# Kernel optimization log

Measured on AMD Instinct MI355X. Metric: run time of the kernel, lower is better.

The kernel has to match this reference:

```python
import jax, jax.numpy as jnp
from jax import lax
import numpy as np


def _lstm_layer(x, W_ih, W_hh, b_ih, b_hh):
    # x: (T, B, in_dim); gate order i, f, g, o (PyTorch convention)
    T, B, _ = x.shape
    H = W_hh.shape[1]
    # precompute input projections for all timesteps (one big GEMM)
    x_proj = jnp.einsum('tbi,gi->tbg', x, W_ih) + b_ih + b_hh  # (T, B, 4H)

    def step(carry, xt):
        h, c = carry
        gates = xt + h @ W_hh.T  # (B, 4H)
        i, f, g, o = jnp.split(gates, 4, axis=-1)
        c = jax.nn.sigmoid(f) * c + jax.nn.sigmoid(i) * jnp.tanh(g)
        h = jax.nn.sigmoid(o) * jnp.tanh(c)
        return (h, c), h

    h0 = jnp.zeros((B, H), dtype=x.dtype)
    c0 = jnp.zeros((B, H), dtype=x.dtype)
    (hT, cT), hs = lax.scan(step, (h0, c0), x_proj)
    return hs, hT, cT


def setup_inputs() -> dict:
    key = jax.random.key(0)
    ks = jax.random.split(key, 12)
    T, B, D_in, H, D_out = 1024, 64, 256, 512, 256
    s_in = 1.0 / np.sqrt(H)
    inp = {
        'x': jax.random.normal(ks[0], (T, B, D_in), jnp.float32),
        'W_ih0': jax.random.uniform(ks[1], (4 * H, D_in), jnp.float32, -s_in, s_in),
        'W_hh0': jax.random.uniform(ks[2], (4 * H, H), jnp.float32, -s_in, s_in),
        'b_ih0': jax.random.uniform(ks[3], (4 * H,), jnp.float32, -s_in, s_in),
        'b_hh0': jax.random.uniform(ks[4], (4 * H,), jnp.float32, -s_in, s_in),
        'W_ih1': jax.random.uniform(ks[5], (4 * H, H), jnp.float32, -s_in, s_in),
        'W_hh1': jax.random.uniform(ks[6], (4 * H, H), jnp.float32, -s_in, s_in),
        'b_ih1': jax.random.uniform(ks[7], (4 * H,), jnp.float32, -s_in, s_in),
        'b_hh1': jax.random.uniform(ks[8], (4 * H,), jnp.float32, -s_in, s_in),
        'W_out': jax.random.uniform(ks[9], (D_out, H), jnp.float32, -s_in, s_in),
        'b_out': jax.random.uniform(ks[10], (D_out,), jnp.float32, -s_in, s_in),
    }
    return inp


def reference(x, W_ih0, W_hh0, b_ih0, b_hh0, W_ih1, W_hh1, b_ih1, b_hh1, W_out, b_out):
    h1s, h1, c1 = _lstm_layer(x, W_ih0, W_hh0, b_ih0, b_hh0)
    h2s, h2, c2 = _lstm_layer(h1s, W_ih1, W_hh1, b_ih1, b_hh1)
    out = jnp.einsum('tbh,oh->tbo', h2s, W_out) + b_out  # (T, B, D_out)
    hn = jnp.stack([h1, h2], axis=0)  # (num_layers, B, H)
    cn = jnp.stack([c1, c2], axis=0)
    return (out, hn, cn)
```

## Files before the change

kernel.cpp:

```cpp
#include <hip/hip_runtime.h>

#define TT   1024
#define BB   64
#define DIN  256
#define HH   512
#define DOUT 256

#define NWG_L0  64
#define NWG_L1  128
#define NWG_OUT 8
#define NWG_TOT 200

typedef short bf16x8 __attribute__((ext_vector_type(8)));
typedef float f32x4  __attribute__((ext_vector_type(4)));
typedef unsigned u32x4 __attribute__((ext_vector_type(4)));

__device__ bf16x8 g_xf[TT * 2048];
__device__ bf16x8 g_h1f[8][4096];
__device__ bf16x8 g_h2f[8][4096];
__device__ bf16x8 g_h1z[4096];
__device__ bf16x8 g_h2z[4096];

__device__ unsigned g_flg[520 * 16];
__device__ unsigned g_iter;

__device__ __forceinline__ unsigned* FLG(int idx) { return &g_flg[idx * 16]; }

__device__ __forceinline__ u32x4 ldg_cv16(const void* p) {
    u32x4 r;
    asm volatile("global_load_dwordx4 %0, %1, off sc0 sc1"
                 : "=&v"(r) : "v"(p) : "memory");
    return r;
}
__device__ __forceinline__ void stg_cv16(void* p, u32x4 v) {
    asm volatile("global_store_dwordx4 %0, %1, off sc0 sc1" :: "v"(p), "v"(v) : "memory");
}
__device__ __forceinline__ void stg_cv_u32(void* p, unsigned v) {
    asm volatile("global_store_dword %0, %1, off sc0 sc1" :: "v"(p), "v"(v) : "memory");
}
__device__ __forceinline__ void wait_vm0(void) {
    asm volatile("s_waitcnt vmcnt(0)" ::: "memory");
}

__device__ __forceinline__ void waitpoll(const unsigned* p, unsigned tgt, int active, int tid) {
    for (;;) {
        unsigned v = 0xFFFFFFFFu;
        if (active)
            asm volatile("global_load_dword %0, %1, off sc0 sc1\n\t"
                         "s_waitcnt vmcnt(0)"
                         : "=&v"(v) : "v"(p) : "memory");
        if (__all(v >= tgt)) break;
        __builtin_amdgcn_s_sleep(1);
    }
    __syncthreads();
}

__device__ __forceinline__ float sigf(float v) { return 1.f / (1.f + __expf(-v)); }
__device__ __forceinline__ float tanh_fast(float v) { return 2.f / (1.f + __expf(-2.f * v)) - 1.f; }

__device__ __forceinline__ short f2bf(float f) {
    unsigned u = __builtin_bit_cast(unsigned, f);
    unsigned r = (u + 0x7FFFu + ((u >> 16) & 1u)) >> 16;
    return (short)r;
}

__device__ __forceinline__ bf16x8 pack8(float4 v0, float4 v1) {
    bf16x8 r;
    r[0] = f2bf(v0.x); r[1] = f2bf(v0.y); r[2] = f2bf(v0.z); r[3] = f2bf(v0.w);
    r[4] = f2bf(v1.x); r[5] = f2bf(v1.y); r[6] = f2bf(v1.z); r[7] = f2bf(v1.w);
    return r;
}

extern "C" __global__ void __launch_bounds__(256)
pack_x(const float* __restrict__ x) {
    const int t = blockIdx.x, tid = threadIdx.x;
    const float* xt = x + (size_t)t * BB * DIN;
    bf16x8* dst = g_xf + (size_t)t * 2048;
    #pragma unroll
    for (int u = 0; u < 8; ++u) {
        const int f = u * 256 + tid;
        const int lane_ = f & 63, ctks = f >> 6;
        const int ct = ctks & 3, ks = ctks >> 2;
        const int b  = ct * 16 + (lane_ & 15);
        const int kb = ks * 32 + (lane_ >> 4) * 8;
        const float4* s = (const float4*)(xt + b * DIN + kb);
        dst[f] = pack8(s[0], s[1]);
    }
}

__device__ void run_l0(int lwg, int tid,
                       const float* __restrict__ wih, const float* __restrict__ whh,
                       const float* __restrict__ bih, const float* __restrict__ bhh,
                       float* __restrict__ out, unsigned Q, bf16x8* sB, short* sH)
{
    constexpr int NCT = 2, NKSA = DIN / 32, NKS = NKSA + HH / 32;
    constexpr int NST = NKS * NCT / 4;
    constexpr int NCXR = NKSA * NCT / 4;

    const int lane = tid & 63, lo = lane & 15, hi = lane >> 4;
    const int w = tid >> 6;
    const int grp = lwg & 1, ub = lwg >> 1;
    const int ctbase = grp * 2;
    const int wv = ub * 4 + w, jbase = wv * 4;
    const int grow = (lo & 3) * HH + jbase + (lo >> 2);

    bf16x8 aF[NKS];
    #pragma unroll
    for (int ks = 0; ks < NKS; ++ks) {
        const float* wr = (ks < NKSA) ? wih + (size_t)grow * DIN + ks * 32 + hi * 8
                                      : whh + (size_t)grow * HH + (ks - NKSA) * 32 + hi * 8;
        const float4* p = (const float4*)wr;
        aF[ks] = pack8(p[0], p[1]);
    }
    f32x4 biasv;
    #pragma unroll
    for (int r = 0; r < 4; ++r)
        biasv[r] = bih[r * HH + jbase + hi] + bhh[r * HH + jbase + hi];

    const unsigned Qb = Q * 2048u;
    float cst[NCT] = {0.f, 0.f};

    for (int t = 0; t < TT; ++t) {
        {
            const unsigned* wp = g_flg; unsigned wt = 0; int wa = 0;
            const int bp = (t >= 8) && ((t & 3) == 0);
            if (w == 0) { if (lane < 32 && t >= 1) { wp = FLG(0 + grp * 32 + lane);
                                                     wt = Qb + t; wa = 1; } }
            else if (w == 1) { if (bp) {
                wp = FLG(192 + (grp * 2 + (lane >> 5)) * 32 + (lane & 31));
                wt = Qb + t - 4; wa = 1; } }
            else if (w == 2) { if (bp && lane < 32) {
                wp = FLG(320 + grp * 32 + lane); wt = Qb + t - 4; wa = 1; } }
            waitpoll(wp, wt, wa, tid);
        }

        const bf16x8* srcA = g_xf + (size_t)t * 2048;
        const bf16x8* srcB = (t == 0) ? g_h1z : g_h1f[(t - 1) & 7];

        u32x4 stg[NST];
        #pragma unroll
        for (int r = 0; r < NST; ++r) {
            const int ri = r * 4 + w, ks = ri / NCT, c = ri % NCT;
            if (r < NCXR) stg[r] = *(const u32x4*)&srcA[(ks * 4 + ctbase + c) * 64 + lane];
            else          stg[r] = ldg_cv16(&srcB[((ks - NKSA) * 4 + ctbase + c) * 64 + lane]);
        }
        wait_vm0();
        #pragma unroll
        for (int r = 0; r < NST; ++r)
            ((u32x4*)sB)[(r * 4 + w) * 64 + lane] = stg[r];
        __syncthreads();
        if (tid == 0) stg_cv_u32(FLG(320 + grp * 32 + ub), Qb + t);

        f32x4 acc[NCT] = {biasv, biasv};
        #pragma unroll
        for (int ks = 0; ks < NKS; ++ks)
            #pragma unroll
            for (int c = 0; c < NCT; ++c)
                acc[c] = __builtin_amdgcn_mfma_f32_16x16x32_bf16(
                    aF[ks], sB[(ks * NCT + c) * 64 + lane], acc[c], 0, 0, 0);

        #pragma unroll
        for (int c = 0; c < NCT; ++c) {
            const float gi = acc[c][0], gf = acc[c][1];
            const float gg = acc[c][2], go = acc[c][3];
            const float cn_ = sigf(gf) * cst[c] + sigf(gi) * tanh_fast(gg);
            const float hv  = sigf(go) * tanh_fast(cn_);
            cst[c] = cn_;
            sH[((c * 2 + (w >> 1)) * 16 + lo) * 8 + (w & 1) * 4 + hi] = f2bf(hv);
            if (t == TT - 1) {
                const int j = jbase + hi, b = (ctbase + c) * 16 + lo;
                const size_t base = (size_t)TT * BB * DOUT;
                out[base + (size_t)b * HH + j] = hv;
                out[base + (size_t)2 * BB * HH + (size_t)b * HH + j] = cn_;
            }
        }
        __syncthreads();

        u32x4* ringW = (u32x4*)g_h1f[t & 7];
        if (tid < 64) {
            const int c = tid >> 5, r = tid & 31, hi2 = r >> 4, lo2 = r & 15;
            const int f = ((ub >> 1) * 4 + ctbase + c) * 64 + ((ub & 1) * 2 + hi2) * 16 + lo2;
            stg_cv16(ringW + f, *(const u32x4*)&sH[((c * 2 + hi2) * 16 + lo2) * 8]);
        }
        wait_vm0();
        if (tid == 0) stg_cv_u32(FLG(0 + grp * 32 + ub), Qb + t + 1);
    }
}

__device__ void run_l1(int lwg, int tid,
                       const float* __restrict__ wih, const float* __restrict__ whh,
                       const float* __restrict__ bih, const float* __restrict__ bhh,
                       float* __restrict__ out, unsigned Q, bf16x8* sB, short* sH)
{
    constexpr int NKSA = HH / 32, NKS = 2 * NKSA;
    constexpr int NSTA = NKSA / 4, NSTB = NKSA / 4;

    const int lane = tid & 63, lo = lane & 15, hi = lane >> 4;
    const int w = tid >> 6;
    const int grp = lwg & 3, ub = lwg >> 2;
    const int ctbase = grp;
    const int wv = ub * 4 + w, jbase = wv * 4;
    const int grow = (lo & 3) * HH + jbase + (lo >> 2);

    bf16x8 aF[NKS];
    #pragma unroll
    for (int ks = 0; ks < NKS; ++ks) {
        const float* wr = (ks < NKSA) ? wih + (size_t)grow * HH + ks * 32 + hi * 8
                                      : whh + (size_t)grow * HH + (ks - NKSA) * 32 + hi * 8;
        const float4* p = (const float4*)wr;
        aF[ks] = pack8(p[0], p[1]);
    }
    f32x4 biasv;
    #pragma unroll
    for (int r = 0; r < 4; ++r)
        biasv[r] = bih[r * HH + jbase + hi] + bhh[r * HH + jbase + hi];

    const unsigned Qb = Q * 2048u;
    float cst = 0.f;

    {
        const unsigned* wp = g_flg; unsigned wt = 0; int wa = 0;
        if (w == 0 && lane < 32) { wp = FLG(0 + (grp >> 1) * 32 + lane); wt = Qb + 1; wa = 1; }
        waitpoll(wp, wt, wa, tid);
    }

    for (int t = 0; t < TT; ++t) {
        const bf16x8* srcA = g_h1f[t & 7];
        const bf16x8* srcB = (t == 0) ? g_h2z : g_h2f[(t - 1) & 7];

        u32x4 stgA[NSTA];
        #pragma unroll
        for (int r = 0; r < NSTA; ++r) {
            const int ks = r * 4 + w;
            stgA[r] = ldg_cv16(&srcA[(ks * 4 + ctbase) * 64 + lane]);
        }
        wait_vm0();
        #pragma unroll
        for (int r = 0; r < NSTA; ++r)
            ((u32x4*)sB)[(r * 4 + w) * 64 + lane] = stgA[r];
        __syncthreads();
        if (tid == 0) stg_cv_u32(FLG(192 + grp * 32 + ub), Qb + t + 1);

        {
            const unsigned* wp = g_flg; unsigned wt = 0; int wa = 0;
            if (w == 0 && lane < 32 && t >= 1) { wp = FLG(64 + grp * 32 + lane);
                                                 wt = Qb + t; wa = 1; }
            waitpoll(wp, wt, wa, tid);
        }

        u32x4 stgB[NSTB];
        #pragma unroll
        for (int r = 0; r < NSTB; ++r) {
            const int ks = r * 4 + w;
            stgB[r] = ldg_cv16(&srcB[(ks * 4 + ctbase) * 64 + lane]);
        }
        f32x4 acc = biasv;
        #pragma unroll
        for (int ks = 0; ks < NKSA; ++ks)
            acc = __builtin_amdgcn_mfma_f32_16x16x32_bf16(
                aF[ks], sB[ks * 64 + lane], acc, 0, 0, 0);
        wait_vm0();
        #pragma unroll
        for (int r = 0; r < NSTB; ++r)
            ((u32x4*)sB)[(NKSA + r * 4 + w) * 64 + lane] = stgB[r];
        __syncthreads();
        if (tid == 0) stg_cv_u32(FLG(384 + grp * 32 + ub), Qb + t);
        #pragma unroll
        for (int ks = NKSA; ks < NKS; ++ks)
            acc = __builtin_amdgcn_mfma_f32_16x16x32_bf16(
                aF[ks], sB[ks * 64 + lane], acc, 0, 0, 0);

        {
            const float gi = acc[0], gf = acc[1], gg = acc[2], go = acc[3];
            const float cn_ = sigf(gf) * cst + sigf(gi) * tanh_fast(gg);
            const float hv  = sigf(go) * tanh_fast(cn_);
            cst = cn_;
            sH[((w >> 1) * 16 + lo) * 8 + (w & 1) * 4 + hi] = f2bf(hv);
            if (t == TT - 1) {
                const int j = jbase + hi, b = ctbase * 16 + lo;
                const size_t base = (size_t)TT * BB * DOUT;
                out[base + (size_t)BB * HH + (size_t)b * HH + j] = hv;
                out[base + (size_t)3 * BB * HH + (size_t)b * HH + j] = cn_;
            }
        }
        __syncthreads();

        u32x4* ringW = (u32x4*)g_h2f[t & 7];
        if (tid < 32) {
            const int hi2 = tid >> 4, lo2 = tid & 15;
            const int f = ((ub >> 1) * 4 + ctbase) * 64 + ((ub & 1) * 2 + hi2) * 16 + lo2;
            stg_cv16(ringW + f, *(const u32x4*)&sH[(hi2 * 16 + lo2) * 8]);
        }
        wait_vm0();
        if (tid == 0) stg_cv_u32(FLG(64 + grp * 32 + ub), Qb + t + 1);

        if (t < TT - 1) {
            const unsigned* wp = g_flg; unsigned wt = 0; int wa = 0;
            const int bp = (t >= 7) && ((t & 3) == 3);
            if (w == 0) { if (lane < 32) { wp = FLG(0 + (grp >> 1) * 32 + lane);
                                           wt = Qb + t + 2; wa = 1; } }
            else if (w == 1) { if (bp) {
                if (lane < 32)      { wp = FLG(384 + grp * 32 + lane);
                                      wt = Qb + t - 3; wa = 1; }
                else if (lane < 36) { wp = FLG(512 + (grp >> 1) * 4 + (lane - 32));
                                      wt = Qb + t - 3; wa = 1; } } }
            waitpoll(wp, wt, wa, tid);
        }
    }
}

__device__ void run_out(int lwg, int tid,
                        const float* __restrict__ wout, const float* __restrict__ bout,
                        float* __restrict__ out, unsigned Q, bf16x8* sB)
{
    constexpr int NKS = HH / 32;
    constexpr int NST = 8;
    const int lane = tid & 63, lo = lane & 15, hi = lane >> 4;
    const int w = tid >> 6;
    const int cp = lwg & 1, ob = lwg >> 1;
    const int ctbase = cp * 2;
    const int obase = (ob * 4 + w) * 16;
    const unsigned Qb = Q * 2048u;

    bf16x8 aF[NKS];
    #pragma unroll
    for (int ks = 0; ks < NKS; ++ks) {
        const float4* p = (const float4*)(wout + (size_t)(obase + lo) * HH + ks * 32 + hi * 8);
        aF[ks] = pack8(p[0], p[1]);
    }
    f32x4 biasv;
    #pragma unroll
    for (int r = 0; r < 4; ++r) biasv[r] = bout[obase + hi * 4 + r];

    for (int t = 0; t < TT; ++t) {
        const unsigned* wp = g_flg; unsigned wt = 0; int wa = 0;
        if (w == 0) {
            wp = FLG(64 + (ctbase + (lane >> 5)) * 32 + (lane & 31));
            wt = Qb + t + 1; wa = 1;
        }
        waitpoll(wp, wt, wa, tid);

        const bf16x8* src = g_h2f[t & 7];
        u32x4 stg[NST];
        #pragma unroll
        for (int r = 0; r < NST; ++r) {
            const int ri = r * 4 + w;
            const int ks = ri >> 1, c = ri & 1;
            stg[r] = ldg_cv16(&src[(ks * 4 + ctbase + c) * 64 + lane]);
        }
        wait_vm0();
        #pragma unroll
        for (int r = 0; r < NST; ++r)
            ((u32x4*)sB)[(r * 4 + w) * 64 + lane] = stg[r];
        __syncthreads();
        if (tid == 0) stg_cv_u32(FLG(512 + cp * 4 + ob), Qb + t + 1);

        f32x4 acc[2] = {biasv, biasv};
        #pragma unroll
        for (int ks = 0; ks < NKS; ++ks)
            #pragma unroll
            for (int c = 0; c < 2; ++c)
                acc[c] = __builtin_amdgcn_mfma_f32_16x16x32_bf16(
                    aF[ks], sB[(ks * 2 + c) * 64 + lane], acc[c], 0, 0, 0);
        #pragma unroll
        for (int c = 0; c < 2; ++c)
            #pragma unroll
            for (int r = 0; r < 4; ++r) {
                const int b = (ctbase + c) * 16 + lo, o = obase + hi * 4 + r;
                out[(size_t)t * BB * DOUT + (size_t)b * DOUT + o] = acc[c][r];
            }
    }
}

extern "C" __global__ void __launch_bounds__(256, 1)
lstm2_fused(const float* __restrict__ x,
            const float* __restrict__ wih0, const float* __restrict__ whh0,
            const float* __restrict__ bih0, const float* __restrict__ bhh0,
            const float* __restrict__ wih1, const float* __restrict__ whh1,
            const float* __restrict__ bih1, const float* __restrict__ bhh1,
            const float* __restrict__ wout, const float* __restrict__ bout,
            float* __restrict__ out)
{
    __shared__ bf16x8 sB[3072];
    __shared__ __align__(16) short sH[2 * 2 * 16 * 8];

    const int tid = threadIdx.x, wg = blockIdx.x;
    const unsigned Q = __hip_atomic_load(&g_iter, __ATOMIC_RELAXED, __HIP_MEMORY_SCOPE_AGENT);

    if (wg < NWG_L0)
        run_l0(wg, tid, wih0, whh0, bih0, bhh0, out, Q, sB, sH);
    else if (wg < NWG_L0 + NWG_L1)
        run_l1(wg - NWG_L0, tid, wih1, whh1, bih1, bhh1, out, Q, sB, sH);
    else
        run_out(wg - NWG_L0 - NWG_L1, tid, wout, bout, out, Q, sB);

    if (wg == 0 && tid == 0)
        __hip_atomic_store(&g_iter, Q + 1, __ATOMIC_RELAXED, __HIP_MEMORY_SCOPE_AGENT);
}

extern "C" void kernel_launch(void* const* d_in, const int* in_sizes, int n_in,
                              void* d_out, int out_size, void* d_ws, size_t ws_size,
                              hipStream_t stream) {
    const float* x    = (const float*)d_in[0];
    const float* wih0 = (const float*)d_in[1];
    const float* whh0 = (const float*)d_in[2];
    const float* bih0 = (const float*)d_in[3];
    const float* bhh0 = (const float*)d_in[4];
    const float* wih1 = (const float*)d_in[5];
    const float* whh1 = (const float*)d_in[6];
    const float* bih1 = (const float*)d_in[7];
    const float* bhh1 = (const float*)d_in[8];
    const float* wout = (const float*)d_in[9];
    const float* bout = (const float*)d_in[10];
    float* out = (float*)d_out;

    hipLaunchKernelGGL(pack_x, dim3(TT), dim3(256), 0, stream, x);
    hipLaunchKernelGGL(lstm2_fused, dim3(NWG_TOT), dim3(256), 0, stream,
                       x, wih0, whh0, bih0, bhh0, wih1, whh1, bih1, bhh1,
                       wout, bout, out);
}
```

Measured before the change: 3.730 ms.

## Shrink h ring to 4 slots and overlap x-projection MFMAs with recurrent loads

Layer 0 now stages its x tile before waiting on the h1 flag and runs the input-projection MFMAs while the recurrent h loads are in flight. Layer 1 moves the h1 staging so wave 0 polls the h2 flag while the other three waves load h1. Both layers drop the trailing __syncthreads and check ring-reuse every step against a 4-slot ring instead of batching the check every 4 steps on an 8-slot ring. The aim is to shorten the serial critical path per timestep, at the cost of tighter producer/consumer coupling and more frequent flag polling.

```diff
diff --git a/kernel.cpp b/kernel.cpp
--- a/kernel.cpp
+++ b/kernel.cpp
@@ -16,8 +16,8 @@
 typedef unsigned u32x4 __attribute__((ext_vector_type(4)));
 
 __device__ bf16x8 g_xf[TT * 2048];
-__device__ bf16x8 g_h1f[8][4096];
-__device__ bf16x8 g_h2f[8][4096];
+__device__ bf16x8 g_h1f[4][4096];
+__device__ bf16x8 g_h2f[4][4096];
 __device__ bf16x8 g_h1z[4096];
 __device__ bf16x8 g_h2z[4096];
 
@@ -93,15 +93,12 @@
                        const float* __restrict__ bih, const float* __restrict__ bhh,
                        float* __restrict__ out, unsigned Q, bf16x8* sB, short* sH)
 {
-    constexpr int NCT = 2, NKSA = DIN / 32, NKS = NKSA + HH / 32;
-    constexpr int NST = NKS * NCT / 4;
-    constexpr int NCXR = NKSA * NCT / 4;
-
+    constexpr int NKSA = 8, NKS = 24;
     const int lane = tid & 63, lo = lane & 15, hi = lane >> 4;
     const int w = tid >> 6;
     const int grp = lwg & 1, ub = lwg >> 1;
     const int ctbase = grp * 2;
-    const int wv = ub * 4 + w, jbase = wv * 4;
+    const int jbase = (ub * 4 + w) * 4;
     const int grow = (lo & 3) * HH + jbase + (lo >> 2);
 
     bf16x8 aF[NKS];
@@ -118,49 +115,58 @@
         biasv[r] = bih[r * HH + jbase + hi] + bhh[r * HH + jbase + hi];
 
     const unsigned Qb = Q * 2048u;
-    float cst[NCT] = {0.f, 0.f};
+    float cst[2] = {0.f, 0.f};
 
     for (int t = 0; t < TT; ++t) {
+        const bf16x8* srcA = g_xf + (size_t)t * 2048;
+        const bf16x8* srcB = (t == 0) ? g_h1z : g_h1f[(t - 1) & 3];
+
+        u32x4 stgA[4];
+        #pragma unroll
+        for (int r = 0; r < 4; ++r) {
+            const int ri = r * 4 + w, ks = ri >> 1, c = ri & 1;
+            stgA[r] = *(const u32x4*)&srcA[(ks * 4 + ctbase + c) * 64 + lane];
+        }
+        wait_vm0();
+        #pragma unroll
+        for (int r = 0; r < 4; ++r)
+            ((u32x4*)sB)[(r * 4 + w) * 64 + lane] = stgA[r];
+
         {
             const unsigned* wp = g_flg; unsigned wt = 0; int wa = 0;
-            const int bp = (t >= 8) && ((t & 3) == 0);
-            if (w == 0) { if (lane < 32 && t >= 1) { wp = FLG(0 + grp * 32 + lane);
-                                                     wt = Qb + t; wa = 1; } }
-            else if (w == 1) { if (bp) {
-                wp = FLG(192 + (grp * 2 + (lane >> 5)) * 32 + (lane & 31));
-                wt = Qb + t - 4; wa = 1; } }
-            else if (w == 2) { if (bp && lane < 32) {
-                wp = FLG(320 + grp * 32 + lane); wt = Qb + t - 4; wa = 1; } }
+            if (w == 0 && lane < 32 && t >= 1) { wp = FLG(0 + grp * 32 + lane);
+                                                 wt = Qb + t; wa = 1; }
             waitpoll(wp, wt, wa, tid);
         }
 
-        const bf16x8* srcA = g_xf + (size_t)t * 2048;
-        const bf16x8* srcB = (t == 0) ? g_h1z : g_h1f[(t - 1) & 7];
-
-        u32x4 stg[NST];
-        #pragma unroll
-        for (int r = 0; r < NST; ++r) {
-            const int ri = r * 4 + w, ks = ri / NCT, c = ri % NCT;
-            if (r < NCXR) stg[r] = *(const u32x4*)&srcA[(ks * 4 + ctbase + c) * 64 + lane];
-            else          stg[r] = ldg_cv16(&srcB[((ks - NKSA) * 4 + ctbase + c) * 64 + lane]);
-        }
-        wait_vm0();
-        #pragma unroll
-        for (int r = 0; r < NST; ++r)
-            ((u32x4*)sB)[(r * 4 + w) * 64 + lane] = stg[r];
+        u32x4 stgB[8];
+        #pragma unroll
+        for (int r = 0; r < 8; ++r) {
+            const int ri = r * 4 + w, ks = ri >> 1, c = ri & 1;
+            stgB[r] = ldg_cv16(&srcB[(ks * 4 + ctbase + c) * 64 + lane]);
+        }
+        f32x4 acc[2] = {biasv, biasv};
+        #pragma unroll
+        for (int ks = 0; ks < NKSA; ++ks)
+            #pragma unroll
+            for (int c = 0; c < 2; ++c)
+                acc[c] = __builtin_amdgcn_mfma_f32_16x16x32_bf16(
+                    aF[ks], sB[(ks * 2 + c) * 64 + lane], acc[c], 0, 0, 0);
+        wait_vm0();
+        #pragma unroll
+        for (int r = 0; r < 8; ++r)
+            ((u32x4*)sB)[(16 + r * 4 + w) * 64 + lane] = stgB[r];
         __syncthreads();
         if (tid == 0) stg_cv_u32(FLG(320 + grp * 32 + ub), Qb + t);
-
-        f32x4 acc[NCT] = {biasv, biasv};
-        #pragma unroll
-        for (int ks = 0; ks < NKS; ++ks)
-            #pragma unroll
-            for (int c = 0; c < NCT; ++c)
+        #pragma unroll
+        for (int ks = NKSA; ks < NKS; ++ks)
+            #pragma unroll
+            for (int c = 0; c < 2; ++c)
                 acc[c] = __builtin_amdgcn_mfma_f32_16x16x32_bf16(
-                    aF[ks], sB[(ks * NCT + c) * 64 + lane], acc[c], 0, 0, 0);
-
-        #pragma unroll
-        for (int c = 0; c < NCT; ++c) {
+                    aF[ks], sB[(ks * 2 + c) * 64 + lane], acc[c], 0, 0, 0);
+
+        #pragma unroll
+        for (int c = 0; c < 2; ++c) {
             const float gi = acc[c][0], gf = acc[c][1];
             const float gg = acc[c][2], go = acc[c][3];
             const float cn_ = sigf(gf) * cst[c] + sigf(gi) * tanh_fast(gg);
@@ -174,9 +180,19 @@
                 out[base + (size_t)2 * BB * HH + (size_t)b * HH + j] = cn_;
             }
         }
-        __syncthreads();
-
-        u32x4* ringW = (u32x4*)g_h1f[t & 7];
+
+        {
+            const unsigned* wp = g_flg; unsigned wt = 0; int wa = 0;
+            if (t >= 4) {
+                if (w == 1) { wp = FLG(192 + (grp * 2 + (lane >> 5)) * 32 + (lane & 31));
+                              wt = Qb + t - 3; wa = 1; }
+                else if (w == 2 && lane < 32) { wp = FLG(320 + grp * 32 + lane);
+                                                wt = Qb + t - 3; wa = 1; }
+            }
+            waitpoll(wp, wt, wa, tid);
+        }
+
+        u32x4* ringW = (u32x4*)g_h1f[t & 3];
         if (tid < 64) {
             const int c = tid >> 5, r = tid & 31, hi2 = r >> 4, lo2 = r & 15;
             const int f = ((ub >> 1) * 4 + ctbase + c) * 64 + ((ub & 1) * 2 + hi2) * 16 + lo2;
@@ -192,14 +208,11 @@
                        const float* __restrict__ bih, const float* __restrict__ bhh,
                        float* __restrict__ out, unsigned Q, bf16x8* sB, short* sH)
 {
-    constexpr int NKSA = HH / 32, NKS = 2 * NKSA;
-    constexpr int NSTA = NKSA / 4, NSTB = NKSA / 4;
-
+    constexpr int NKSA = 16, NKS = 32;
     const int lane = tid & 63, lo = lane & 15, hi = lane >> 4;
     const int w = tid >> 6;
     const int grp = lwg & 3, ub = lwg >> 2;
-    const int ctbase = grp;
-    const int wv = ub * 4 + w, jbase = wv * 4;
+    const int jbase = (ub * 4 + w) * 4;
     const int grow = (lo & 3) * HH + jbase + (lo >> 2);
 
     bf16x8 aF[NKS];
@@ -218,41 +231,53 @@
     const unsigned Qb = Q * 2048u;
     float cst = 0.f;
 
-    {
-        const unsigned* wp = g_flg; unsigned wt = 0; int wa = 0;
-        if (w == 0 && lane < 32) { wp = FLG(0 + (grp >> 1) * 32 + lane); wt = Qb + 1; wa = 1; }
-        waitpoll(wp, wt, wa, tid);
-    }
-
     for (int t = 0; t < TT; ++t) {
-        const bf16x8* srcA = g_h1f[t & 7];
-        const bf16x8* srcB = (t == 0) ? g_h2z : g_h2f[(t - 1) & 7];
-
-        u32x4 stgA[NSTA];
-        #pragma unroll
-        for (int r = 0; r < NSTA; ++r) {
-            const int ks = r * 4 + w;
-            stgA[r] = ldg_cv16(&srcA[(ks * 4 + ctbase) * 64 + lane]);
-        }
-        wait_vm0();
-        #pragma unroll
-        for (int r = 0; r < NSTA; ++r)
-            ((u32x4*)sB)[(r * 4 + w) * 64 + lane] = stgA[r];
+        const bf16x8* srcA = g_h1f[t & 3];
+        const bf16x8* srcB = (t == 0) ? g_h2z : g_h2f[(t - 1) & 3];
+
+        {
+            const unsigned* wp = g_flg; unsigned wt = 0; int wa = 0;
+            if (w == 0 && lane < 32) { wp = FLG(0 + (grp >> 1) * 32 + lane);
+                                       wt = Qb + t + 1; wa = 1; }
+            waitpoll(wp, wt, wa, tid);
+        }
+
+        if (w == 0) {
+            if (t >= 1) {
+                const unsigned* p = FLG(64 + grp * 32 + lane);
+                const unsigned tgt = Qb + t;
+                for (;;) {
+                    unsigned v = 0xFFFFFFFFu;
+                    if (lane < 32)
+                        asm volatile("global_load_dword %0, %1, off sc0 sc1\n\t"
+                                     "s_waitcnt vmcnt(0)"
+                                     : "=&v"(v) : "v"(p) : "memory");
+                    if (__all(v >= tgt)) break;
+                    __builtin_amdgcn_s_sleep(1);
+                }
+            }
+        } else {
+            u32x4 sa[6];
+            #pragma unroll
+            for (int r = 0; r < 6; ++r) {
+                const int ri = r * 3 + (w - 1);
+                if (ri < 16) sa[r] = ldg_cv16(&srcA[(ri * 4 + grp) * 64 + lane]);
+            }
+            wait_vm0();
+            #pragma unroll
+            for (int r = 0; r < 6; ++r) {
+                const int ri = r * 3 + (w - 1);
+                if (ri < 16) ((u32x4*)sB)[ri * 64 + lane] = sa[r];
+            }
+        }
         __syncthreads();
         if (tid == 0) stg_cv_u32(FLG(192 + grp * 32 + ub), Qb + t + 1);
 
-        {
-            const unsigned* wp = g_flg; unsigned wt = 0; int wa = 0;
-            if (w == 0 && lane < 32 && t >= 1) { wp = FLG(64 + grp * 32 + lane);
-                                                 wt = Qb + t; wa = 1; }
-            waitpoll(wp, wt, wa, tid);
-        }
-
-        u32x4 stgB[NSTB];
-        #pragma unroll
-        for (int r = 0; r < NSTB; ++r) {
+        u32x4 sb[4];
+        #pragma unroll
+        for (int r = 0; r < 4; ++r) {
             const int ks = r * 4 + w;
-            stgB[r] = ldg_cv16(&srcB[(ks * 4 + ctbase) * 64 + lane]);
+            sb[r] = ldg_cv16(&srcB[(ks * 4 + grp) * 64 + lane]);
         }
         f32x4 acc = biasv;
         #pragma unroll
@@ -261,8 +286,8 @@
                 aF[ks], sB[ks * 64 + lane], acc, 0, 0, 0);
         wait_vm0();
         #pragma unroll
-        for (int r = 0; r < NSTB; ++r)
-            ((u32x4*)sB)[(NKSA + r * 4 + w) * 64 + lane] = stgB[r];
+        for (int r = 0; r < 4; ++r)
+            ((u32x4*)sB)[(16 + r * 4 + w) * 64 + lane] = sb[r];
         __syncthreads();
         if (tid == 0) stg_cv_u32(FLG(384 + grp * 32 + ub), Qb + t);
         #pragma unroll
@@ -277,35 +302,32 @@
             cst = cn_;
             sH[((w >> 1) * 16 + lo) * 8 + (w & 1) * 4 + hi] = f2bf(hv);
             if (t == TT - 1) {
-                const int j = jbase + hi, b = ctbase * 16 + lo;
+                const int j = jbase + hi, b = grp * 16 + lo;
                 const size_t base = (size_t)TT * BB * DOUT;
                 out[base + (size_t)BB * HH + (size_t)b * HH + j] = hv;
                 out[base + (size_t)3 * BB * HH + (size_t)b * HH + j] = cn_;
             }
         }
-        __syncthreads();
-
-        u32x4* ringW = (u32x4*)g_h2f[t & 7];
-        if (tid < 32) {
-            const int hi2 = tid >> 4, lo2 = tid & 15;
-            const int f = ((ub >> 1) * 4 + ctbase) * 64 + ((ub & 1) * 2 + hi2) * 16 + lo2;
-            stg_cv16(ringW + f, *(const u32x4*)&sH[(hi2 * 16 + lo2) * 8]);
-        }
-        wait_vm0();
-        if (tid == 0) stg_cv_u32(FLG(64 + grp * 32 + ub), Qb + t + 1);
-
-        if (t < TT - 1) {
+
+        {
             const unsigned* wp = g_flg; unsigned wt = 0; int wa = 0;
-            const int bp = (t >= 7) && ((t & 3) == 3);
-            if (w == 0) { if (lane < 32) { wp = FLG(0 + (grp >> 1) * 32 + lane);
-                                           wt = Qb + t + 2; wa = 1; } }
-            else if (w == 1) { if (bp) {
+            if (t >= 4 && w == 1) {
                 if (lane < 32)      { wp = FLG(384 + grp * 32 + lane);
                                       wt = Qb + t - 3; wa = 1; }
                 else if (lane < 36) { wp = FLG(512 + (grp >> 1) * 4 + (lane - 32));
-                                      wt = Qb + t - 3; wa = 1; } } }
+                                      wt = Qb + t - 3; wa = 1; }
+            }
             waitpoll(wp, wt, wa, tid);
         }
+
+        u32x4* ringW = (u32x4*)g_h2f[t & 3];
+        if (tid < 32) {
+            const int hi2 = tid >> 4, lo2 = tid & 15;
+            const int f = ((ub >> 1) * 4 + grp) * 64 + ((ub & 1) * 2 + hi2) * 16 + lo2;
+            stg_cv16(ringW + f, *(const u32x4*)&sH[(hi2 * 16 + lo2) * 8]);
+        }
+        wait_vm0();
+        if (tid == 0) stg_cv_u32(FLG(64 + grp * 32 + ub), Qb + t + 1);
     }
 }
 
@@ -340,7 +362,7 @@
         }
         waitpoll(wp, wt, wa, tid);
 
-        const bf16x8* src = g_h2f[t & 7];
+        const bf16x8* src = g_h2f[t & 3];
         u32x4 stg[NST];
         #pragma unroll
         for (int r = 0; r < NST; ++r) {
```

Result: slower. 3.814 ms (+2.3%).
